# Kernel tuning notes

Measured on AMD Instinct MI355X. Metric: run time of the kernel, lower is better.

## Reference

```python
import jax, jax.numpy as jnp
import numpy as np
import math

DIM = 512


def setup_inputs() -> dict:
    key = jax.random.key(0)
    ks = jax.random.split(key, 6)
    B, N, D = 4, 4096, DIM
    H = D // 2
    features = jax.random.normal(ks[0], (B, N, D), dtype=jnp.float32)
    W1 = jax.random.normal(ks[1], (D, H), dtype=jnp.float32) * 0.02
    b1 = jnp.zeros((H,), dtype=jnp.float32)
    ln_g = jnp.ones((H,), dtype=jnp.float32)
    ln_b = jnp.zeros((H,), dtype=jnp.float32)
    W2 = jax.random.normal(ks[2], (H, 1), dtype=jnp.float32) * 0.02
    b2 = jnp.zeros((1,), dtype=jnp.float32)
    target_entropy = jnp.ones((1,), dtype=jnp.float32) * math.log(D)
    temperature = jnp.ones((1,), dtype=jnp.float32)
    return {"features": features, "W1": W1, "b1": b1, "ln_g": ln_g,
            "ln_b": ln_b, "W2": W2, "b2": b2,
            "target_entropy": target_entropy, "temperature": temperature}


def _layernorm(x, g, b, eps=1e-5):
    mu = jnp.mean(x, axis=-1, keepdims=True)
    var = jnp.mean((x - mu) ** 2, axis=-1, keepdims=True)
    return (x - mu) * jax.lax.rsqrt(var + eps) * g + b


def reference(features, W1, b1, ln_g, ln_b, W2, b2, target_entropy, temperature):
    # ---- compute_entropy: pairwise RBF kernel over [B, N, D] ----
    sq = jnp.sum(features ** 2, axis=-1)                       # [B, N]
    gram = jnp.einsum('bnd,bmd->bnm', features, features)      # [B, N, N]
    d2 = jnp.maximum(sq[:, :, None] + sq[:, None, :] - 2.0 * gram, 0.0)
    tau = temperature[0]
    kernel = jnp.exp(-d2 / (2.0 * tau ** 2))                   # [B, N, N]
    probs = kernel / jnp.sum(kernel, axis=-1, keepdims=True)
    entropy = -jnp.sum(probs * jnp.log(probs + 1e-6), axis=-1)  # [B, N]

    # ---- entropy estimator MLP (computed in original forward, output unused) ----
    h = features @ W1 + b1
    h = _layernorm(h, ln_g, ln_b)
    h = jax.nn.gelu(h, approximate=False)
    estimated_entropy = h @ W2 + b2                            # [B, N, 1] (unused)
    del estimated_entropy

    # ---- sigmoid-gated control signal ----
    entropy_diff = entropy - target_entropy[0]
    control_signal = jax.nn.sigmoid(-entropy_diff / tau)       # [B, N]
    controlled_features = features * control_signal[..., None]
    return controlled_features, control_signal
```

## Files before the change

kernel.cpp:

```cpp
#include <hip/hip_runtime.h>
#include <stdint.h>

#define N_TOK 4096
#define DIM   512
#define BATCH 4
#define BN    (BATCH * N_TOK)
#define JSPLIT 8
#define IPW   64
#define IPB   256
#define NG    (N_TOK / JSPLIT / 16)
#define SPG   4
#define NSP   (NG / SPG)

typedef __attribute__((ext_vector_type(4))) float f32x4;
typedef __attribute__((ext_vector_type(8))) int   i32x8;

typedef const __attribute__((address_space(1))) uint32_t* gptr_t;
typedef __attribute__((address_space(3))) uint32_t* lptr_t;

__device__ __forceinline__ float sumsq8(uint lo, uint hi) {
    float s = 0.f, f;
    f = __builtin_amdgcn_cvt_f32_fp8((int)lo, 0); s = fmaf(f, f, s);
    f = __builtin_amdgcn_cvt_f32_fp8((int)lo, 1); s = fmaf(f, f, s);
    f = __builtin_amdgcn_cvt_f32_fp8((int)lo, 2); s = fmaf(f, f, s);
    f = __builtin_amdgcn_cvt_f32_fp8((int)lo, 3); s = fmaf(f, f, s);
    f = __builtin_amdgcn_cvt_f32_fp8((int)hi, 0); s = fmaf(f, f, s);
    f = __builtin_amdgcn_cvt_f32_fp8((int)hi, 1); s = fmaf(f, f, s);
    f = __builtin_amdgcn_cvt_f32_fp8((int)hi, 2); s = fmaf(f, f, s);
    f = __builtin_amdgcn_cvt_f32_fp8((int)hi, 3); s = fmaf(f, f, s);
    return s;
}

__global__ __launch_bounds__(256) void prep_kernel(
    const float* __restrict__ feat, uint8_t* __restrict__ fbT,
    float* __restrict__ sq)
{
    __shared__ __align__(16) long lt[1024];
    const int t = threadIdx.x;
    const int row16 = t >> 4, seg = t & 15;
    const size_t grp = blockIdx.x;
    const size_t row = grp * 16 + row16;

    const float4* src = (const float4*)(feat + row * DIM + seg * 32);
    uint32_t wd[8];
    float s = 0.f;
#pragma unroll
    for (int i = 0; i < 4; ++i) {
        float4 a = src[2 * i], b = src[2 * i + 1];
        uint lo = (uint)__builtin_amdgcn_cvt_pk_fp8_f32(a.x, a.y, 0, false);
        lo      = (uint)__builtin_amdgcn_cvt_pk_fp8_f32(a.z, a.w, (int)lo, true);
        uint hi = (uint)__builtin_amdgcn_cvt_pk_fp8_f32(b.x, b.y, 0, false);
        hi      = (uint)__builtin_amdgcn_cvt_pk_fp8_f32(b.z, b.w, (int)hi, true);
        wd[2 * i] = lo; wd[2 * i + 1] = hi;
        s += sumsq8(lo, hi);
    }

#pragma unroll
    for (int i = 0; i < 4; ++i) {
        int c = seg * 4 + i;
        long d = ((long)(unsigned)wd[2 * i + 1] << 32) | (unsigned)wd[2 * i];
        lt[c * 16 + ((row16 + c) & 15)] = d;
    }

#pragma unroll
    for (int m = 1; m < 16; m <<= 1) s += __shfl_xor(s, m);
    if (seg == 0) sq[row] = s;

    __syncthreads();
    long* ot = (long*)(fbT + grp * 8192);
#pragma unroll
    for (int i = 0; i < 4; ++i) {
        int p    = t + i * 256;
        int kk   = p >> 8;
        int rem  = p & 255;
        int half = rem >> 7;
        int l6   = (rem >> 1) & 63;
        int qq   = l6 >> 4;
        int r    = l6 & 15;
        int w8   = half * 2 + (p & 1);
        int c    = kk * 16 + qq * 4 + w8;
        ot[p] = lt[c * 16 + ((r + c) & 15)];
    }
}

__global__ __launch_bounds__(256, 2) void entropy_kernel(
    const uint8_t* __restrict__ fbT,
    const float* __restrict__ sq, const float* __restrict__ temp,
    float* __restrict__ Sp, float* __restrict__ Tp)
{
    __shared__ uint4 buf[2][2048];
    __shared__ float sqlds[NG * 16];
    const int t    = threadIdx.x;
    const int w    = t >> 6;
    const int lane = t & 63;
    const int q    = lane >> 4;
    const int c16  = lane & 15;
    const int lbo  = lane * 16;

    const int flat  = blockIdx.x;
    const int combo = flat & 31;
    const int batch = combo >> 3;
    const int jh    = combo & 7;
    const int iblk  = flat >> 5;
    const int iw    = iblk * IPB + w * IPW;
    const size_t rowbase = (size_t)batch * N_TOK;

    const float tau    = temp[0];
    const float inv2t2 = 0.5f / (tau * tau);
    const float cg_    = 1.0f / (tau * tau);

    i32x8 afrag[4][4];
#pragma unroll
    for (int s = 0; s < 4; ++s) {
        const uint8_t* ga = fbT + ((rowbase + iw) / 16 + s) * 8192;
#pragma unroll
        for (int kk = 0; kk < 4; ++kk) {
            uint4 lo = *(const uint4*)(ga + kk * 2048 + lbo);
            uint4 hi = *(const uint4*)(ga + kk * 2048 + 1024 + lbo);
            i32x8 v = {(int)lo.x, (int)lo.y, (int)lo.z, (int)lo.w,
                       (int)hi.x, (int)hi.y, (int)hi.z, (int)hi.w};
            afrag[s][kk] = v;
        }
    }
    float pi_[4][4];
    float pim = -1e30f;
#pragma unroll
    for (int s = 0; s < 4; ++s) {
        float4 p4 = *(const float4*)(sq + rowbase + iw + s * 16 + q * 4);
        pi_[s][0] = -p4.x * inv2t2; pi_[s][1] = -p4.y * inv2t2;
        pi_[s][2] = -p4.z * inv2t2; pi_[s][3] = -p4.w * inv2t2;
        pim = fmaxf(pim, fmaxf(fmaxf(pi_[s][0], pi_[s][1]),
                               fmaxf(pi_[s][2], pi_[s][3])));
    }
    {
        const float* sqslice = sq + rowbase + (size_t)jh * (N_TOK / JSPLIT);
        sqlds[t]       = sqslice[t];
        sqlds[t + 256] = sqslice[t + 256];
    }

    float S[4][4], T[4][4];
#pragma unroll
    for (int s = 0; s < 4; ++s)
#pragma unroll
        for (int r = 0; r < 4; ++r) { S[s][r] = 0.f; T[s][r] = 0.f; }

    const uint8_t* bgbase = fbT
        + ((size_t)batch * (N_TOK / 16) + (size_t)jh * NG) * 8192;

    auto stage_sp = [&](int sp, int b) {
#pragma unroll
        for (int i = 0; i < SPG; ++i) {
            const uint8_t* gs = bgbase + ((size_t)sp * SPG + i) * 8192 + w * 2048 + lbo;
            uint8_t* ld = (uint8_t*)(&buf[b][0]) + i * 8192 + w * 2048;
            __builtin_amdgcn_global_load_lds((gptr_t)(const void*)gs,
                                             (lptr_t)(void*)ld, 16, 0, 0);
            __builtin_amdgcn_global_load_lds((gptr_t)(const void*)(gs + 1024),
                                             (lptr_t)(void*)(ld + 1024), 16, 0, 0);
        }
    };

    stage_sp(0, 0);
    stage_sp(1, 1);
    asm volatile("s_waitcnt lgkmcnt(0)" ::: "memory");
    __builtin_amdgcn_s_barrier();

    for (int sp = 0; sp < NSP; ++sp) {
        if (sp < NSP - 1) asm volatile("s_waitcnt vmcnt(8)" ::: "memory");
        else              asm volatile("s_waitcnt vmcnt(0)" ::: "memory");
        __builtin_amdgcn_s_barrier();
        __builtin_amdgcn_sched_barrier(0);

        const uint8_t* sb = (const uint8_t*)(&buf[sp & 1][0]);
        __builtin_amdgcn_s_setprio(1);
#pragma unroll
        for (int i = 0; i < SPG; ++i) {
            const int g = sp * SPG + i;
            const uint8_t* bs = sb + i * 8192;
            float pj = -sqlds[g * 16 + c16] * inv2t2;
            f32x4 acc[4] = {{0,0,0,0},{0,0,0,0},{0,0,0,0},{0,0,0,0}};
#pragma unroll
            for (int kk = 0; kk < 4; ++kk) {
                uint4 lo = *(const uint4*)(bs + kk * 2048 + lbo);
                uint4 hi = *(const uint4*)(bs + kk * 2048 + 1024 + lbo);
                i32x8 b = {(int)lo.x, (int)lo.y, (int)lo.z, (int)lo.w,
                           (int)hi.x, (int)hi.y, (int)hi.z, (int)hi.w};
                acc[0] = __builtin_amdgcn_mfma_scale_f32_16x16x128_f8f6f4(afrag[0][kk], b, acc[0], 0, 0, 0, 127, 0, 127);
                acc[1] = __builtin_amdgcn_mfma_scale_f32_16x16x128_f8f6f4(afrag[1][kk], b, acc[1], 0, 0, 0, 127, 0, 127);
                acc[2] = __builtin_amdgcn_mfma_scale_f32_16x16x128_f8f6f4(afrag[2][kk], b, acc[2], 0, 0, 0, 127, 0, 127);
                acc[3] = __builtin_amdgcn_mfma_scale_f32_16x16x128_f8f6f4(afrag[3][kk], b, acc[3], 0, 0, 0, 127, 0, 127);
            }
            float m0 = fmaxf(fmaxf(acc[0][0], acc[0][1]), fmaxf(acc[0][2], acc[0][3]));
            float m1 = fmaxf(fmaxf(acc[1][0], acc[1][1]), fmaxf(acc[1][2], acc[1][3]));
            float m2 = fmaxf(fmaxf(acc[2][0], acc[2][1]), fmaxf(acc[2][2], acc[2][3]));
            float m3 = fmaxf(fmaxf(acc[3][0], acc[3][1]), fmaxf(acc[3][2], acc[3][3]));
            float mm = fmaxf(fmaxf(m0, m1), fmaxf(m2, m3));
            float bound = fmaf(mm, cg_, pim + pj);
            if (bound > -110.0f) {
#pragma unroll
                for (int s = 0; s < 4; ++s)
#pragma unroll
                    for (int r = 0; r < 4; ++r) {
                        float e  = fmaf(acc[s][r], cg_, pi_[s][r] + pj);
                        float ee = fminf(e, 0.f);
                        float k  = __expf(ee);
                        S[s][r] += k;
                        T[s][r]  = fmaf(k, ee, T[s][r]);
                    }
            }
        }
        __builtin_amdgcn_s_setprio(0);

        asm volatile("s_waitcnt lgkmcnt(0)" ::: "memory");
        __builtin_amdgcn_s_barrier();
        __builtin_amdgcn_sched_barrier(0);
        if (sp + 2 < NSP) stage_sp(sp + 2, sp & 1);
    }

#pragma unroll
    for (int m = 1; m < 16; m <<= 1)
#pragma unroll
        for (int s = 0; s < 4; ++s)
#pragma unroll
            for (int r = 0; r < 4; ++r) {
                S[s][r] += __shfl_xor(S[s][r], m);
                T[s][r] += __shfl_xor(T[s][r], m);
            }

    if (c16 == 0) {
#pragma unroll
        for (int s = 0; s < 4; ++s)
#pragma unroll
            for (int r = 0; r < 4; ++r) {
                size_t idx = (size_t)jh * BN + rowbase + iw + s * 16 + q * 4 + r;
                Sp[idx] = S[s][r];
                Tp[idx] = T[s][r];
            }
    }
}

__global__ __launch_bounds__(256) void finalize_kernel(
    const float* __restrict__ feat, const float* __restrict__ Sp,
    const float* __restrict__ Tp, const float* __restrict__ tgt,
    const float* __restrict__ temp, float* __restrict__ out)
{
    int row  = (blockIdx.x << 2) + (threadIdx.x >> 6);
    int lane = threadIdx.x & 63;
    float S = 0.0f, T = 0.0f;
#pragma unroll
    for (int j = 0; j < JSPLIT; ++j) {
        S += Sp[(size_t)j * BN + row];
        T += Tp[(size_t)j * BN + row];
    }
    float tau = temp[0];
    float E  = __logf(S) - T / S;
    float cs = 1.0f / (1.0f + __expf((E - tgt[0]) / tau));

    const float4* F4 = (const float4*)(feat + (size_t)row * DIM);
    float4*       O4 = (float4*)(out + (size_t)row * DIM);
    float4 v0 = F4[lane], v1 = F4[lane + 64];
    v0.x *= cs; v0.y *= cs; v0.z *= cs; v0.w *= cs;
    v1.x *= cs; v1.y *= cs; v1.z *= cs; v1.w *= cs;
    O4[lane] = v0; O4[lane + 64] = v1;
    if (lane == 0) out[(size_t)BN * DIM + row] = cs;
}

extern "C" void kernel_launch(void* const* d_in, const int* in_sizes, int n_in,
                              void* d_out, int out_size, void* d_ws, size_t ws_size,
                              hipStream_t stream) {
    const float* feat = (const float*)d_in[0];
    const float* tgt  = (const float*)d_in[7];
    const float* temp = (const float*)d_in[8];
    float* out = (float*)d_out;

    char* ws = (char*)d_ws;
    uint8_t* fbT = (uint8_t*)ws;
    float*   sq  = (float*)(fbT + (size_t)BN * DIM);
    float*   Sp  = sq + BN;
    float*   Tp  = Sp + (size_t)JSPLIT * BN;

    prep_kernel<<<dim3(BN / 16), dim3(256), 0, stream>>>(feat, fbT, sq);
    entropy_kernel<<<dim3((N_TOK / IPB) * BATCH * JSPLIT), dim3(256), 0, stream>>>(fbT, sq, temp, Sp, Tp);
    finalize_kernel<<<dim3(BN / 4), dim3(256), 0, stream>>>(feat, Sp, Tp, tgt, temp, out);
}
```

Before: 143.9 us.

## Exploit Gram matrix symmetry by computing only upper-triangular 256x256 tile pairs

The pairwise kernel is symmetric, so each block now handles one (i-tile, j-tile) pair with i<=j, 136 pairs per batch instead of the full grid. Off-diagonal blocks also reduce kernel sums along columns through shuffles and shared memory and write them as partial sums for the j rows. This roughly halves the MFMA and exp work. In exchange it adds column reductions, extra shared memory, a serial pair-index decode loop, and twice as many partial slices for finalize to read. The skip test also becomes wave-uniform via __any, so whole waves skip or compute together.

```diff
diff --git a/kernel.cpp b/kernel.cpp
--- a/kernel.cpp
+++ b/kernel.cpp
@@ -5,12 +5,13 @@
 #define DIM   512
 #define BATCH 4
 #define BN    (BATCH * N_TOK)
-#define JSPLIT 8
+#define NSUP  16
+#define NPAIR 136
 #define IPW   64
 #define IPB   256
-#define NG    (N_TOK / JSPLIT / 16)
-#define SPG   4
-#define NSP   (NG / SPG)
+#define NG2   16
+#define SPG   2
+#define NSP   (NG2 / SPG)
 
 typedef __attribute__((ext_vector_type(4))) float f32x4;
 typedef __attribute__((ext_vector_type(8))) int   i32x8;
@@ -88,8 +89,10 @@
     const float* __restrict__ sq, const float* __restrict__ temp,
     float* __restrict__ Sp, float* __restrict__ Tp)
 {
-    __shared__ uint4 buf[2][2048];
-    __shared__ float sqlds[NG * 16];
+    __shared__ uint4 buf[2][1024];
+    __shared__ float sqlds[256];
+    __shared__ float sjS[4][256];
+    __shared__ float sjT[4][256];
     const int t    = threadIdx.x;
     const int w    = t >> 6;
     const int lane = t & 63;
@@ -98,16 +101,21 @@
     const int lbo  = lane * 16;
 
     const int flat  = blockIdx.x;
-    const int combo = flat & 31;
-    const int batch = combo >> 3;
-    const int jh    = combo & 7;
-    const int iblk  = flat >> 5;
-    const int iw    = iblk * IPB + w * IPW;
+    const int batch = flat / NPAIR;
+    int rem = flat - batch * NPAIR;
+    int aa = 0;
+    while (rem >= NSUP - aa) { rem -= NSUP - aa; ++aa; }
+    const int bb = aa + rem;
+    const int iw    = aa * IPB + w * IPW;
+    const int jbase = bb * IPB;
     const size_t rowbase = (size_t)batch * N_TOK;
 
     const float tau    = temp[0];
     const float inv2t2 = 0.5f / (tau * tau);
     const float cg_    = 1.0f / (tau * tau);
+
+#pragma unroll
+    for (int i = 0; i < 4; ++i) { sjS[w][lane * 4 + i] = 0.f; sjT[w][lane * 4 + i] = 0.f; }
 
     i32x8 afrag[4][4];
 #pragma unroll
@@ -132,11 +140,7 @@
         pim = fmaxf(pim, fmaxf(fmaxf(pi_[s][0], pi_[s][1]),
                                fmaxf(pi_[s][2], pi_[s][3])));
     }
-    {
-        const float* sqslice = sq + rowbase + (size_t)jh * (N_TOK / JSPLIT);
-        sqlds[t]       = sqslice[t];
-        sqlds[t + 256] = sqslice[t + 256];
-    }
+    sqlds[t] = sq[rowbase + jbase + t];
 
     float S[4][4], T[4][4];
 #pragma unroll
@@ -145,7 +149,7 @@
         for (int r = 0; r < 4; ++r) { S[s][r] = 0.f; T[s][r] = 0.f; }
 
     const uint8_t* bgbase = fbT
-        + ((size_t)batch * (N_TOK / 16) + (size_t)jh * NG) * 8192;
+        + ((size_t)batch * (N_TOK / 16) + (size_t)(jbase / 16)) * 8192;
 
     auto stage_sp = [&](int sp, int b) {
 #pragma unroll
@@ -165,7 +169,7 @@
     __builtin_amdgcn_s_barrier();
 
     for (int sp = 0; sp < NSP; ++sp) {
-        if (sp < NSP - 1) asm volatile("s_waitcnt vmcnt(8)" ::: "memory");
+        if (sp < NSP - 1) asm volatile("s_waitcnt vmcnt(4)" ::: "memory");
         else              asm volatile("s_waitcnt vmcnt(0)" ::: "memory");
         __builtin_amdgcn_s_barrier();
         __builtin_amdgcn_sched_barrier(0);
@@ -195,17 +199,27 @@
             float m3 = fmaxf(fmaxf(acc[3][0], acc[3][1]), fmaxf(acc[3][2], acc[3][3]));
             float mm = fmaxf(fmaxf(m0, m1), fmaxf(m2, m3));
             float bound = fmaf(mm, cg_, pim + pj);
-            if (bound > -110.0f) {
+            if (__any(bound > -110.0f)) {
+                float ks = 0.f, kt = 0.f;
 #pragma unroll
                 for (int s = 0; s < 4; ++s)
 #pragma unroll
                     for (int r = 0; r < 4; ++r) {
-                        float e  = fmaf(acc[s][r], cg_, pi_[s][r] + pj);
-                        float ee = fminf(e, 0.f);
-                        float k  = __expf(ee);
-                        S[s][r] += k;
-                        T[s][r]  = fmaf(k, ee, T[s][r]);
+                        float e   = fmaf(acc[s][r], cg_, pi_[s][r] + pj);
+                        float ee  = fminf(e, 0.f);
+                        float k   = __expf(ee);
+                        float kei = k * ee;
+                        S[s][r] += k;  T[s][r] += kei;
+                        ks      += k;  kt      += kei;
                     }
+                if (aa != bb) {
+                    ks += __shfl_xor(ks, 16); ks += __shfl_xor(ks, 32);
+                    kt += __shfl_xor(kt, 16); kt += __shfl_xor(kt, 32);
+                    if (lane < 16) {
+                        sjS[w][g * 16 + lane] = ks;
+                        sjT[w][g * 16 + lane] = kt;
+                    }
+                }
             }
         }
         __builtin_amdgcn_s_setprio(0);
@@ -225,16 +239,24 @@
                 S[s][r] += __shfl_xor(S[s][r], m);
                 T[s][r] += __shfl_xor(T[s][r], m);
             }
-
     if (c16 == 0) {
 #pragma unroll
         for (int s = 0; s < 4; ++s)
 #pragma unroll
             for (int r = 0; r < 4; ++r) {
-                size_t idx = (size_t)jh * BN + rowbase + iw + s * 16 + q * 4 + r;
+                size_t idx = (size_t)bb * BN + rowbase + iw + s * 16 + q * 4 + r;
                 Sp[idx] = S[s][r];
                 Tp[idx] = T[s][r];
             }
+    }
+
+    if (aa != bb) {
+        __syncthreads();
+        float s4 = sjS[0][t] + sjS[1][t] + sjS[2][t] + sjS[3][t];
+        float t4 = sjT[0][t] + sjT[1][t] + sjT[2][t] + sjT[3][t];
+        size_t idx = (size_t)aa * BN + rowbase + jbase + t;
+        Sp[idx] = s4;
+        Tp[idx] = t4;
     }
 }
 
@@ -247,7 +269,7 @@
     int lane = threadIdx.x & 63;
     float S = 0.0f, T = 0.0f;
 #pragma unroll
-    for (int j = 0; j < JSPLIT; ++j) {
+    for (int j = 0; j < NSUP; ++j) {
         S += Sp[(size_t)j * BN + row];
         T += Tp[(size_t)j * BN + row];
     }
@@ -276,9 +298,9 @@
     uint8_t* fbT = (uint8_t*)ws;
     float*   sq  = (float*)(fbT + (size_t)BN * DIM);
     float*   Sp  = sq + BN;
-    float*   Tp  = Sp + (size_t)JSPLIT * BN;
+    float*   Tp  = Sp + (size_t)NSUP * BN;
 
     prep_kernel<<<dim3(BN / 16), dim3(256), 0, stream>>>(feat, fbT, sq);
-    entropy_kernel<<<dim3((N_TOK / IPB) * BATCH * JSPLIT), dim3(256), 0, stream>>>(fbT, sq, temp, Sp, Tp);
+    entropy_kernel<<<dim3(BATCH * NPAIR), dim3(256), 0, stream>>>(fbT, sq, temp, Sp, Tp);
     finalize_kernel<<<dim3(BN / 4), dim3(256), 0, stream>>>(feat, Sp, Tp, tgt, temp, out);
 }
```

Result: faster. 139.7 us (-2.9%).
